# Kernel tuning notes

Measured on AMD Instinct MI355X. Metric: run time of the kernel, lower is better.

## Reference

```python
import jax, jax.numpy as jnp
import numpy as np

B, T, H = 16, 512, 1024
L, D = 8192, 256

def setup_inputs() -> dict:
    key = jax.random.key(0)
    k1, k2, k3, k4, k5 = jax.random.split(key, 5)
    X = jax.random.normal(k1, (B, T, H), dtype=jnp.float32)
    attention_mask = jnp.ones((B, T), dtype=jnp.int32)
    queries = jax.random.normal(k2, (L, D), dtype=jnp.float32) * 0.02
    Wk = jax.random.normal(k3, (D, H), dtype=jnp.float32) * (1.0 / np.sqrt(H))
    Wv = jax.random.normal(k4, (D, H), dtype=jnp.float32) * (1.0 / np.sqrt(H))
    out_weight = jax.random.normal(k5, (L, D), dtype=jnp.float32) * 0.02
    out_bias = jnp.zeros((L,), dtype=jnp.float32)
    return {"X": X, "attention_mask": attention_mask, "queries": queries,
            "Wk": Wk, "Wv": Wv, "out_weight": out_weight, "out_bias": out_bias}

def reference(X, attention_mask, queries, Wk, Wv, out_weight, out_bias):
    # K, V: [B, T, D] (nn.Linear with weight [D, H], no bias)
    K = jnp.einsum('bth,dh->btd', X, Wk)
    V = jnp.einsum('bth,dh->btd', X, Wv)
    scale = 1.0 / jnp.sqrt(jnp.asarray(K.shape[-1], dtype=K.dtype))
    # attention logits: [B, L, T]
    attn_logits = jnp.einsum('ld,btd->blt', queries, K) * scale
    neg = jnp.finfo(attn_logits.dtype).min
    attn_logits = jnp.where(attention_mask[:, None, :] == 0, neg, attn_logits)
    attn = jax.nn.softmax(attn_logits, axis=-1)
    # per-label context: [B, L, D]
    ctx = jnp.einsum('blt,btd->bld', attn, V)
    # fused per-label output projection: [B, L]
    logits = jnp.einsum('bld,ld->bl', ctx, out_weight) + out_bias[None, :]
    return logits
```

## Files before the change

### kernel.cpp

```cpp
#include <hip/hip_runtime.h>
#include <hip/hip_bf16.h>


typedef __bf16 bf16x8 __attribute__((ext_vector_type(8)));
typedef float f32x4 __attribute__((ext_vector_type(4)));

__device__ __forceinline__ unsigned short f2bf(float f) {
    unsigned int u = __builtin_bit_cast(unsigned int, f);
    unsigned int lsb = (u >> 16) & 1u;
    u += 0x7fffu + lsb;
    return (unsigned short)(u >> 16);
}

__device__ __forceinline__ void gld_lds16(const void* g, void* l) {
    __builtin_amdgcn_global_load_lds((__attribute__((address_space(1))) void*)g,
                                     (__attribute__((address_space(3))) void*)l,
                                     16, 0, 0);
}

__global__ __launch_bounds__(256) void cvt_all(const float* __restrict__ X,
                                               const float* __restrict__ Q,
                                               const float* __restrict__ Wo,
                                               const float* __restrict__ Wk,
                                               const float* __restrict__ Wv,
                                               unsigned short* __restrict__ dst) {
    int base = blockIdx.x * 1024 + threadIdx.x;
#pragma unroll
    for (int r = 0; r < 4; ++r) {
        int idx = base + r * 256;
        const float* src;
        int off;
        float s = 1.0f;
        if (idx < 2097152)      { src = X;  off = idx; }
        else if (idx < 2621440) { src = Q;  off = idx - 2097152; s = 0.0625f; }
        else if (idx < 3145728) { src = Wo; off = idx - 2621440; }
        else if (idx < 3211264) { src = Wk; off = idx - 3145728; }
        else                    { src = Wv; off = idx - 3211264; }
        float4 v = ((const float4*)src)[off];
        ushort4 o;
        o.x = f2bf(v.x * s); o.y = f2bf(v.y * s);
        o.z = f2bf(v.z * s); o.w = f2bf(v.w * s);
        ((ushort4*)dst)[idx] = o;
    }
}

__global__ __launch_bounds__(256) void kv_gemm(const unsigned short* __restrict__ Xb,
                                               const unsigned short* __restrict__ Wb,
                                               unsigned short* __restrict__ Kb,
                                               unsigned short* __restrict__ Vb) {
    __shared__ unsigned short Xs[128 * 72];
    __shared__ unsigned short Ws[128 * 72];
    const int bid = blockIdx.x;
    const int nt = bid & 3, mt = bid >> 2;
    const int m0 = mt * 128, n0 = nt * 128;
    const int tid = threadIdx.x;
    const int lane = tid & 63, w = tid >> 6;
    const int q = lane >> 4, ln = lane & 15;
    const int wm = (w & 1) * 64, wn = (w >> 1) * 64;

    f32x4 acc[4][4];
#pragma unroll
    for (int mi = 0; mi < 4; ++mi)
#pragma unroll
        for (int ni = 0; ni < 4; ++ni) acc[mi][ni] = f32x4{0.f, 0.f, 0.f, 0.f};

#pragma unroll 1
    for (int h0 = 0; h0 < 1024; h0 += 64) {
#pragma unroll
        for (int i = 0; i < 4; ++i) {
            int c = tid + i * 256;
            int row = c >> 3, off = (c & 7) << 3;
            *(uint4*)(&Xs[row * 72 + off]) = *(const uint4*)(&Xb[(m0 + row) * 1024 + h0 + off]);
            *(uint4*)(&Ws[row * 72 + off]) = *(const uint4*)(&Wb[(n0 + row) * 1024 + h0 + off]);
        }
        __syncthreads();
#pragma unroll
        for (int ks = 0; ks < 64; ks += 32) {
            bf16x8 a[4], b[4];
#pragma unroll
            for (int mi = 0; mi < 4; ++mi)
                a[mi] = *(const bf16x8*)(&Xs[(wm + mi * 16 + ln) * 72 + ks + q * 8]);
#pragma unroll
            for (int ni = 0; ni < 4; ++ni)
                b[ni] = *(const bf16x8*)(&Ws[(wn + ni * 16 + ln) * 72 + ks + q * 8]);
#pragma unroll
            for (int mi = 0; mi < 4; ++mi)
#pragma unroll
                for (int ni = 0; ni < 4; ++ni)
                    acc[mi][ni] = __builtin_amdgcn_mfma_f32_16x16x32_bf16(
                        a[mi], b[ni], acc[mi][ni], 0, 0, 0);
        }
        __syncthreads();
    }
    {
        unsigned short* dst = (n0 < 256) ? Kb : Vb;
        const int d0 = (n0 & 255) + wn;
#pragma unroll
        for (int mi = 0; mi < 4; ++mi)
#pragma unroll
            for (int ni = 0; ni < 4; ++ni) {
                int d = d0 + ni * 16 + ln;
#pragma unroll
                for (int r = 0; r < 4; ++r) {
                    int m = m0 + wm + mi * 16 + q * 4 + r;
                    dst[m * 256 + d] = f2bf(acc[mi][ni][r]);
                }
            }
    }
}

__global__ __launch_bounds__(256, 2) void attn_fused(const unsigned short* __restrict__ Qb,
                                                     const unsigned short* __restrict__ Wob,
                                                     const unsigned short* __restrict__ Kb,
                                                     const unsigned short* __restrict__ Vb,
                                                     const int* __restrict__ mask,
                                                     const float* __restrict__ bias,
                                                     float* __restrict__ out) {
    __shared__ unsigned short Ks[2][8320];
    __shared__ unsigned short Vs[2][8320];
    const int bid = blockIdx.x;
    const int bb = bid >> 6;
    const int l0 = (bid & 63) * 128;
    const int tid = threadIdx.x;
    const int lane = tid & 63, w = tid >> 6;
    const int q = lane >> 4, ln = lane & 15;
    const int laneoff = ((lane >> 3) * 32) + (((lane >> 2) & 1) * 256) + ((lane & 3) * 8);

    unsigned mbits = 0;
    {
        const int* mrow = mask + bb * 512;
#pragma unroll
        for (int j = 0; j < 32; ++j)
            mbits |= (mrow[j * 16 + ln] != 0 ? 1u : 0u) << j;
    }

    bf16x8 aQ[2][8], aW[2][8];
#pragma unroll
    for (int mi = 0; mi < 2; ++mi) {
        const int row = (l0 + w * 32 + mi * 16 + ln) * 256;
#pragma unroll
        for (int kk = 0; kk < 8; ++kk) {
            aQ[mi][kk] = *(const bf16x8*)(&Qb[row + kk * 32 + q * 8]);
            aW[mi][kk] = *(const bf16x8*)(&Wob[row + kk * 32 + q * 8]);
        }
    }

    float num[2][4], den[2][4];
#pragma unroll
    for (int mi = 0; mi < 2; ++mi)
#pragma unroll
        for (int r = 0; r < 4; ++r) { num[mi][r] = 0.f; den[mi][r] = 0.f; }

    auto stage = [&](int c) {
        const int p = c & 1;
        const int rbase = bb * 512 + c * 32;
#pragma unroll
        for (int j = 0; j < 8; ++j) {
            int gid = w * 8 + j;
            int g = gid & 15;
            const unsigned short* srcb = (gid < 16) ? Kb : Vb;
            unsigned short* dstb = (gid < 16) ? &Ks[p][0] : &Vs[p][0];
            gld_lds16(srcb + (((size_t)(rbase + 2 * g)) << 8) + laneoff,
                      dstb + g * 520);
        }
    };
    stage(0);

#pragma unroll 1
    for (int c = 0; c < 16; ++c) {
        __syncthreads();
        if (c < 15) stage(c + 1);
        const int p = c & 1;

        f32x4 Sa[2][2], Pa[2][2];
#pragma unroll
        for (int mi = 0; mi < 2; ++mi)
#pragma unroll
            for (int ni = 0; ni < 2; ++ni) {
                Sa[mi][ni] = f32x4{0.f, 0.f, 0.f, 0.f};
                Pa[mi][ni] = f32x4{0.f, 0.f, 0.f, 0.f};
            }

#pragma unroll
        for (int kk = 0; kk < 8; ++kk) {
            bf16x8 bK[2], bV[2];
#pragma unroll
            for (int ni = 0; ni < 2; ++ni) {
                int rr = ni * 16 + ln;
                int off = (rr >> 1) * 520 + kk * 64 + (rr & 1) * 32 + q * 8;
                bK[ni] = *(const bf16x8*)(&Ks[p][off]);
                bV[ni] = *(const bf16x8*)(&Vs[p][off]);
            }
#pragma unroll
            for (int mi = 0; mi < 2; ++mi)
#pragma unroll
                for (int ni = 0; ni < 2; ++ni) {
                    Sa[mi][ni] = __builtin_amdgcn_mfma_f32_16x16x32_bf16(
                        aQ[mi][kk], bK[ni], Sa[mi][ni], 0, 0, 0);
                    Pa[mi][ni] = __builtin_amdgcn_mfma_f32_16x16x32_bf16(
                        aW[mi][kk], bV[ni], Pa[mi][ni], 0, 0, 0);
                }
        }
#pragma unroll
        for (int ni = 0; ni < 2; ++ni) {
            bool ok = (mbits >> (c * 2 + ni)) & 1u;
#pragma unroll
            for (int mi = 0; mi < 2; ++mi)
#pragma unroll
                for (int r = 0; r < 4; ++r) {
                    float e = ok ? __expf(Sa[mi][ni][r]) : 0.0f;
                    den[mi][r] += e;
                    num[mi][r] += e * Pa[mi][ni][r];
                }
        }
    }

#pragma unroll
    for (int mi = 0; mi < 2; ++mi)
#pragma unroll
        for (int r = 0; r < 4; ++r) {
            float n_ = num[mi][r], d_ = den[mi][r];
#pragma unroll
            for (int o = 1; o < 16; o <<= 1) {
                n_ += __shfl_xor(n_, o);
                d_ += __shfl_xor(d_, o);
            }
            if (ln == 0) {
                int l = l0 + w * 32 + mi * 16 + q * 4 + r;
                out[bb * 8192 + l] = n_ / d_ + bias[l];
            }
        }
}

extern "C" void kernel_launch(void* const* d_in, const int* in_sizes, int n_in,
                              void* d_out, int out_size, void* d_ws, size_t ws_size,
                              hipStream_t stream) {
    const float* X    = (const float*)d_in[0];
    const int*   mask = (const int*)d_in[1];
    const float* Q    = (const float*)d_in[2];
    const float* Wk   = (const float*)d_in[3];
    const float* Wv   = (const float*)d_in[4];
    const float* Wo   = (const float*)d_in[5];
    const float* bias = (const float*)d_in[6];
    float* out = (float*)d_out;

    unsigned short* Xb   = (unsigned short*)d_ws;
    unsigned short* Qb   = Xb + 8388608ull;
    unsigned short* Wob  = Qb + 2097152ull;
    unsigned short* Wkvb = Wob + 2097152ull;
    unsigned short* Kb   = Wkvb + 524288ull;
    unsigned short* Vb   = Kb + 2097152ull;

    cvt_all<<<dim3(3200), 256, 0, stream>>>(X, Q, Wo, Wk, Wv, Xb);
    kv_gemm<<<dim3(256), 256, 0, stream>>>(Xb, Wkvb, Kb, Vb);
    attn_fused<<<dim3(1024), 256, 0, stream>>>(Qb, Wob, Kb, Vb, mask, bias, out);
}
```

Measured before the change: 194.0 us.

## Double-buffer kv_gemm with direct global-to-LDS loads and smaller M tiles

The K/V projection GEMM now stages X and W tiles into double-buffered LDS using global_load_lds, so the next k-slice loads while MFMAs run on the current one, and one barrier per iteration is removed. The M tile shrinks from 128 to 64, doubling the grid to 512 blocks, and the launch bounds allow two blocks per CU. This targets poor latency hiding and low CU occupancy on a 256-block launch. In exchange each block reuses less data, and the LDS layout changes to an 8-row-group format without padding, which may cause bank conflicts.

```diff
diff --git a/kernel.cpp b/kernel.cpp
--- a/kernel.cpp
+++ b/kernel.cpp
@@ -44,65 +44,80 @@
     }
 }
 
-__global__ __launch_bounds__(256) void kv_gemm(const unsigned short* __restrict__ Xb,
-                                               const unsigned short* __restrict__ Wb,
-                                               unsigned short* __restrict__ Kb,
-                                               unsigned short* __restrict__ Vb) {
-    __shared__ unsigned short Xs[128 * 72];
-    __shared__ unsigned short Ws[128 * 72];
+__global__ __launch_bounds__(256, 2) void kv_gemm(const unsigned short* __restrict__ Xb,
+                                                  const unsigned short* __restrict__ Wb,
+                                                  unsigned short* __restrict__ Kb,
+                                                  unsigned short* __restrict__ Vb) {
+    __shared__ unsigned short Xs[2][8 * 512];
+    __shared__ unsigned short Ws[2][16 * 512];
     const int bid = blockIdx.x;
     const int nt = bid & 3, mt = bid >> 2;
-    const int m0 = mt * 128, n0 = nt * 128;
+    const int m0 = mt * 64, n0 = nt * 128;
     const int tid = threadIdx.x;
     const int lane = tid & 63, w = tid >> 6;
     const int q = lane >> 4, ln = lane & 15;
-    const int wm = (w & 1) * 64, wn = (w >> 1) * 64;
-
-    f32x4 acc[4][4];
+    const int lh = ln >> 3, ls = ln & 7;
+    const int sub = lane & 7, ech = lane >> 3;
+
+    f32x4 acc[4][2];
 #pragma unroll
     for (int mi = 0; mi < 4; ++mi)
 #pragma unroll
-        for (int ni = 0; ni < 4; ++ni) acc[mi][ni] = f32x4{0.f, 0.f, 0.f, 0.f};
+        for (int ni = 0; ni < 2; ++ni) acc[mi][ni] = f32x4{0.f, 0.f, 0.f, 0.f};
+
+    auto stage = [&](int it) {
+        const int p = it & 1;
+        const int h0 = it * 64;
+#pragma unroll
+        for (int j = 0; j < 6; ++j) {
+            int gid = w * 6 + j;
+            if (gid < 8) {
+                gld_lds16(Xb + (size_t)(m0 + 8 * gid + sub) * 1024 + h0 + ech * 8,
+                          &Xs[p][gid * 512]);
+            } else {
+                int g = gid - 8;
+                gld_lds16(Wb + (size_t)(n0 + 8 * g + sub) * 1024 + h0 + ech * 8,
+                          &Ws[p][g * 512]);
+            }
+        }
+    };
+    stage(0);
 
 #pragma unroll 1
-    for (int h0 = 0; h0 < 1024; h0 += 64) {
-#pragma unroll
-        for (int i = 0; i < 4; ++i) {
-            int c = tid + i * 256;
-            int row = c >> 3, off = (c & 7) << 3;
-            *(uint4*)(&Xs[row * 72 + off]) = *(const uint4*)(&Xb[(m0 + row) * 1024 + h0 + off]);
-            *(uint4*)(&Ws[row * 72 + off]) = *(const uint4*)(&Wb[(n0 + row) * 1024 + h0 + off]);
-        }
+    for (int it = 0; it < 16; ++it) {
         __syncthreads();
-#pragma unroll
-        for (int ks = 0; ks < 64; ks += 32) {
-            bf16x8 a[4], b[4];
+        if (it < 15) stage(it + 1);
+        const int p = it & 1;
+#pragma unroll
+        for (int kb = 0; kb < 2; ++kb) {
+            bf16x8 a[4], b[2];
 #pragma unroll
             for (int mi = 0; mi < 4; ++mi)
-                a[mi] = *(const bf16x8*)(&Xs[(wm + mi * 16 + ln) * 72 + ks + q * 8]);
-#pragma unroll
-            for (int ni = 0; ni < 4; ++ni)
-                b[ni] = *(const bf16x8*)(&Ws[(wn + ni * 16 + ln) * 72 + ks + q * 8]);
+                a[mi] = *(const bf16x8*)(
+                    &Xs[p][(2 * mi + lh) * 512 + ls * 8 + (q + 4 * kb) * 64]);
+#pragma unroll
+            for (int ni = 0; ni < 2; ++ni)
+                b[ni] = *(const bf16x8*)(
+                    &Ws[p][(4 * w + 2 * ni + lh) * 512 + ls * 8 + (q + 4 * kb) * 64]);
 #pragma unroll
             for (int mi = 0; mi < 4; ++mi)
 #pragma unroll
-                for (int ni = 0; ni < 4; ++ni)
+                for (int ni = 0; ni < 2; ++ni)
                     acc[mi][ni] = __builtin_amdgcn_mfma_f32_16x16x32_bf16(
                         a[mi], b[ni], acc[mi][ni], 0, 0, 0);
         }
-        __syncthreads();
     }
     {
         unsigned short* dst = (n0 < 256) ? Kb : Vb;
-        const int d0 = (n0 & 255) + wn;
+        const int d0 = (n0 & 255) + w * 32;
 #pragma unroll
         for (int mi = 0; mi < 4; ++mi)
 #pragma unroll
-            for (int ni = 0; ni < 4; ++ni) {
+            for (int ni = 0; ni < 2; ++ni) {
                 int d = d0 + ni * 16 + ln;
 #pragma unroll
                 for (int r = 0; r < 4; ++r) {
-                    int m = m0 + wm + mi * 16 + q * 4 + r;
+                    int m = m0 + mi * 16 + q * 4 + r;
                     dst[m * 256 + d] = f2bf(acc[mi][ni][r]);
                 }
             }
@@ -252,6 +267,6 @@
     unsigned short* Vb   = Kb + 2097152ull;
 
     cvt_all<<<dim3(3200), 256, 0, stream>>>(X, Q, Wo, Wk, Wv, Xb);
-    kv_gemm<<<dim3(256), 256, 0, stream>>>(Xb, Wkvb, Kb, Vb);
+    kv_gemm<<<dim3(512), 256, 0, stream>>>(Xb, Wkvb, Kb, Vb);
     attn_fused<<<dim3(1024), 256, 0, stream>>>(Qb, Wob, Kb, Vb, mask, bias, out);
 }
```

After: 197.2 us. No clear change (+1.7%).

## Halve key/value chunk size to cut LDS and allow three blocks per CU

Applied to the files above, without the earlier changes.

Shrinks each staged K/V chunk from 32 to 16 sequence rows, halving LDS buffers and per-iteration accumulator registers, and raises the launch bound to 3 blocks per CU. The intent is higher occupancy to better hide load latency. In exchange the loop runs twice as many iterations with twice as many barriers and smaller MFMA batches per sync.

```diff
diff --git a/kernel.cpp b/kernel.cpp
--- a/kernel.cpp
+++ b/kernel.cpp
@@ -109,15 +109,15 @@
     }
 }
 
-__global__ __launch_bounds__(256, 2) void attn_fused(const unsigned short* __restrict__ Qb,
+__global__ __launch_bounds__(256, 3) void attn_fused(const unsigned short* __restrict__ Qb,
                                                      const unsigned short* __restrict__ Wob,
                                                      const unsigned short* __restrict__ Kb,
                                                      const unsigned short* __restrict__ Vb,
                                                      const int* __restrict__ mask,
                                                      const float* __restrict__ bias,
                                                      float* __restrict__ out) {
-    __shared__ unsigned short Ks[2][8320];
-    __shared__ unsigned short Vs[2][8320];
+    __shared__ unsigned short Ks[2][4160];
+    __shared__ unsigned short Vs[2][4160];
     const int bid = blockIdx.x;
     const int bb = bid >> 6;
     const int l0 = (bid & 63) * 128;
@@ -153,13 +153,13 @@
 
     auto stage = [&](int c) {
         const int p = c & 1;
-        const int rbase = bb * 512 + c * 32;
-#pragma unroll
-        for (int j = 0; j < 8; ++j) {
-            int gid = w * 8 + j;
-            int g = gid & 15;
-            const unsigned short* srcb = (gid < 16) ? Kb : Vb;
-            unsigned short* dstb = (gid < 16) ? &Ks[p][0] : &Vs[p][0];
+        const int rbase = bb * 512 + c * 16;
+#pragma unroll
+        for (int j = 0; j < 4; ++j) {
+            int gid = w * 4 + j;
+            int g = gid & 7;
+            const unsigned short* srcb = (gid < 8) ? Kb : Vb;
+            unsigned short* dstb = (gid < 8) ? &Ks[p][0] : &Vs[p][0];
             gld_lds16(srcb + (((size_t)(rbase + 2 * g)) << 8) + laneoff,
                       dstb + g * 520);
         }
@@ -167,52 +167,40 @@
     stage(0);
 
 #pragma unroll 1
-    for (int c = 0; c < 16; ++c) {
+    for (int c = 0; c < 32; ++c) {
         __syncthreads();
-        if (c < 15) stage(c + 1);
+        if (c < 31) stage(c + 1);
         const int p = c & 1;
 
-        f32x4 Sa[2][2], Pa[2][2];
+        f32x4 Sa[2], Pa[2];
+#pragma unroll
+        for (int mi = 0; mi < 2; ++mi) {
+            Sa[mi] = f32x4{0.f, 0.f, 0.f, 0.f};
+            Pa[mi] = f32x4{0.f, 0.f, 0.f, 0.f};
+        }
+
+#pragma unroll
+        for (int kk = 0; kk < 8; ++kk) {
+            int off = (ln >> 1) * 520 + kk * 64 + (ln & 1) * 32 + q * 8;
+            bf16x8 bK = *(const bf16x8*)(&Ks[p][off]);
+            bf16x8 bV = *(const bf16x8*)(&Vs[p][off]);
+#pragma unroll
+            for (int mi = 0; mi < 2; ++mi) {
+                Sa[mi] = __builtin_amdgcn_mfma_f32_16x16x32_bf16(
+                    aQ[mi][kk], bK, Sa[mi], 0, 0, 0);
+                Pa[mi] = __builtin_amdgcn_mfma_f32_16x16x32_bf16(
+                    aW[mi][kk], bV, Pa[mi], 0, 0, 0);
+            }
+        }
+        bool ok = (mbits >> c) & 1u;
 #pragma unroll
         for (int mi = 0; mi < 2; ++mi)
 #pragma unroll
-            for (int ni = 0; ni < 2; ++ni) {
-                Sa[mi][ni] = f32x4{0.f, 0.f, 0.f, 0.f};
-                Pa[mi][ni] = f32x4{0.f, 0.f, 0.f, 0.f};
-            }
-
-#pragma unroll
-        for (int kk = 0; kk < 8; ++kk) {
-            bf16x8 bK[2], bV[2];
-#pragma unroll
-            for (int ni = 0; ni < 2; ++ni) {
-                int rr = ni * 16 + ln;
-                int off = (rr >> 1) * 520 + kk * 64 + (rr & 1) * 32 + q * 8;
-                bK[ni] = *(const bf16x8*)(&Ks[p][off]);
-                bV[ni] = *(const bf16x8*)(&Vs[p][off]);
-            }
-#pragma unroll
-            for (int mi = 0; mi < 2; ++mi)
-#pragma unroll
-                for (int ni = 0; ni < 2; ++ni) {
-                    Sa[mi][ni] = __builtin_amdgcn_mfma_f32_16x16x32_bf16(
-                        aQ[mi][kk], bK[ni], Sa[mi][ni], 0, 0, 0);
-                    Pa[mi][ni] = __builtin_amdgcn_mfma_f32_16x16x32_bf16(
-                        aW[mi][kk], bV[ni], Pa[mi][ni], 0, 0, 0);
-                }
-        }
-#pragma unroll
-        for (int ni = 0; ni < 2; ++ni) {
-            bool ok = (mbits >> (c * 2 + ni)) & 1u;
-#pragma unroll
-            for (int mi = 0; mi < 2; ++mi)
-#pragma unroll
-                for (int r = 0; r < 4; ++r) {
-                    float e = ok ? __expf(Sa[mi][ni][r]) : 0.0f;
-                    den[mi][r] += e;
-                    num[mi][r] += e * Pa[mi][ni][r];
-                }
-        }
+            for (int r = 0; r < 4; ++r) {
+                float e = ok ? __expf(Sa[mi][r]) : 0.0f;
+                den[mi][r] += e;
+                num[mi][r] += e * Pa[mi][r];
+            }
     }
 
 #pragma unroll
```

Result: slower. 260.6 us (+34.4%).
